# Kernel optimization log

Hardware: AMD Instinct MI355X
Metric: run time of the kernel (lower is better)

## Reference

```python
import jax, jax.numpy as jnp
import numpy as np

# pywt db8 reconstruction low-pass filter (rec_lo); other filters derived per pywt conventions
_REC_LO = np.array([
    0.05441584224308161, 0.3128715909144659, 0.6756307362980128,
    0.5853546836548691, -0.015829105256023893, -0.2840155429624281,
    0.00047248457399797254, 0.128747426620186, -0.01736930100202211,
    -0.04408825393106472, 0.013981027917015516, 0.008746094047015655,
    -0.00487035299301066, -0.0003917403729959771, 0.0006754494059985568,
    -0.00011747678400228192], dtype=np.float64)
_F = 16
_REC_HI = np.array([(-1.0) ** k * _REC_LO[_F - 1 - k] for k in range(_F)])  # qmf
_DEC_LO = _REC_LO[::-1].copy()
_DEC_HI = _REC_HI[::-1].copy()
# lax.conv does cross-correlation; np.convolve flips the filter, so pre-flip here
_DEC_K = np.ascontiguousarray(np.stack([_DEC_LO[::-1], _DEC_HI[::-1]])[:, None, :])  # [2,1,F]
_REC_K = np.ascontiguousarray(np.stack([_REC_LO[::-1], _REC_HI[::-1]])[None, :, :])  # [1,2,F]
_THRESHOLD_FACTOR = 1.0


def _dwt_last(x):
    # single-level DWT along last axis, pywt 'symmetric' boundary mode
    shp = x.shape
    xf = x.reshape(-1, 1, shp[-1])
    xe = jnp.pad(xf, ((0, 0), (0, 0), (_F - 1, _F - 1)), mode='symmetric')[:, :, 1:]
    y = jax.lax.conv_general_dilated(xe, jnp.asarray(_DEC_K, x.dtype), (2,), 'VALID',
                                     dimension_numbers=('NCW', 'OIW', 'NCW'))  # [M,2,n]
    n = y.shape[-1]  # n = floor((N + F - 1) / 2)
    return y[:, 0].reshape(shp[:-1] + (n,)), y[:, 1].reshape(shp[:-1] + (n,))


def _idwt_last(ca, cd, out_len):
    # single-level inverse DWT along last axis; out_len = 2*n - F + 2
    shp = ca.shape
    n = shp[-1]
    m = int(np.prod(shp[:-1]))
    u = jnp.zeros((m, 2, 2 * n), ca.dtype)
    u = u.at[:, 0, ::2].set(ca.reshape(m, n)).at[:, 1, ::2].set(cd.reshape(m, n))
    ue = jnp.pad(u, ((0, 0), (0, 0), (_F - 1, _F - 1)))
    y = jax.lax.conv_general_dilated(ue, jnp.asarray(_REC_K, ca.dtype), (1,), 'VALID',
                                     dimension_numbers=('NCW', 'OIW', 'NCW'))[:, 0]
    return y[:, _F - 2:_F - 2 + out_len].reshape(shp[:-1] + (out_len,))


def _forward(x):
    B, H, W, C = x.shape
    M = B * C
    xm = jnp.transpose(x, (0, 3, 1, 2)).reshape(M, H, W)
    # level-1 wavedec2: rows (W axis) then columns (H axis)
    lo, hi = _dwt_last(xm)                               # [M,H,nW]
    ll, lh = _dwt_last(jnp.swapaxes(lo, -1, -2))         # [M,nW,nH]
    hl, hh = _dwt_last(jnp.swapaxes(hi, -1, -2))         # [M,nW,nH]
    # universal threshold from median abs of all detail subbands, per sample/channel
    det = jnp.concatenate([lh.reshape(M, -1), hl.reshape(M, -1), hh.reshape(M, -1)], axis=-1)
    sigma = jnp.median(jnp.abs(det), axis=-1) / 0.6745
    t = (sigma * jnp.sqrt(2.0 * jnp.log(float(H * W))) * _THRESHOLD_FACTOR)[:, None, None]
    soft = lambda c: jnp.sign(c) * jnp.maximum(jnp.abs(c) - t, 0.0)
    lh, hl, hh = soft(lh), soft(hl), soft(hh)
    # waverec2: inverse along H then along W
    nH = ll.shape[-1]
    Hr = 2 * nH - _F + 2
    rl = jnp.swapaxes(_idwt_last(ll, lh, Hr), -1, -2)    # [M,Hr,nW]
    rh = jnp.swapaxes(_idwt_last(hl, hh, Hr), -1, -2)    # [M,Hr,nW]
    nW = rl.shape[-1]
    y = _idwt_last(rl, rh, 2 * nW - _F + 2)              # [M,Hr,Wr]
    y = y[:, :H, :W].reshape(B, C, H, W)
    return jnp.transpose(y, (0, 2, 3, 1)).astype(x.dtype)


def setup_inputs() -> dict:
    key = jax.random.key(0)
    x = jax.random.normal(key, (32, 512, 512, 3), dtype=jnp.float32)
    return {"x": x}


def reference(x):
    return _forward(x)
```

## Files before the change

kernel.cpp:

```cpp
#include <hip/hip_runtime.h>
#include <math.h>

#define B_   32
#define H_   512
#define W_   512
#define C_   3
#define M_   96
#define NW_  263
#define NH_  263
#define DETPER 69169
#define DETTOT 207507
#define DETSTRIDE 207508
#define NVEC 51876
#define KRANK  103753u

#define SXS 144
#define CR  12

#define CAP  32768
#define LCAP 4096

__device__ __constant__ float RLO[16] = {
    0.05441584224308161f,  0.3128715909144659f,   0.6756307362980128f,
    0.5853546836548691f,  -0.015829105256023893f, -0.2840155429624281f,
    0.00047248457399797254f, 0.128747426620186f,  -0.01736930100202211f,
   -0.04408825393106472f,  0.013981027917015516f,  0.008746094047015655f,
   -0.00487035299301066f, -0.0003917403729959771f, 0.0006754494059985568f,
   -0.00011747678400228192f};
__device__ __constant__ float RHI[16] = {
   -0.00011747678400228192f, -0.0006754494059985568f, -0.0003917403729959771f,
    0.00487035299301066f,     0.008746094047015655f,  -0.013981027917015516f,
   -0.04408825393106472f,     0.01736930100202211f,    0.128747426620186f,
   -0.00047248457399797254f, -0.2840155429624281f,     0.015829105256023893f,
    0.5853546836548691f,     -0.6756307362980128f,     0.3128715909144659f,
   -0.05441584224308161f};

__device__ __forceinline__ int refl(int q, int N) {
    if (q < 0)  return -q - 1;
    if (q >= N) return 2 * N - 1 - q;
    return q;
}

__device__ __forceinline__ float softthr(float v, float thr) {
    float a = fabsf(v) - thr;
    return a > 0.f ? copysignf(a, v) : 0.f;
}

__global__ __launch_bounds__(256) void k_zero(unsigned* __restrict__ p, int n) {
    int i = blockIdx.x * 256 + threadIdx.x;
    if (i < n) p[i] = 0u;
}

__global__ __launch_bounds__(256) void k_fwd(const float* __restrict__ x,
                                             float* __restrict__ ll,
                                             float* __restrict__ det,
                                             unsigned* __restrict__ hist) {
    __shared__ float sX[CR * SXS];
    __shared__ float sLO[46 * 64], sHI[46 * 64];
    __shared__ unsigned hh[2048];
    const int m   = blockIdx.x;
    const int jw0 = blockIdx.y * 64;
    const int jh0 = blockIdx.z * 16;
    const int b = m / 3, c = m - 3 * (m / 3);
    const int tid = threadIdx.x;
    const int prow0 = 2 * jh0 - 14, pcol0 = 2 * jw0 - 14;
    for (int i = tid; i < 2048; i += 256) hh[i] = 0u;
    for (int r0 = 0; r0 < 46; r0 += CR) {
        const int nr = (46 - r0) < CR ? (46 - r0) : CR;
        for (int l = tid; l < nr * 142; l += 256) {
            int rr = l / 142, cl = l - rr * 142;
            int h = refl(prow0 + r0 + rr, H_);
            int w = refl(pcol0 + cl, W_);
            sX[rr * SXS + cl] = x[((size_t)(b * H_ + h) * W_ + w) * C_ + c];
        }
        __syncthreads();
        for (int l = tid; l < nr * 64; l += 256) {
            int rr = l >> 6, j = l & 63;
            const float* px = &sX[rr * SXS + 2 * j];
            float al = 0.f, ah = 0.f;
#pragma unroll
            for (int k = 0; k < 16; ++k) {
                al = fmaf(px[k], RLO[k], al);
                ah = fmaf(px[k], RHI[k], ah);
            }
            sLO[(r0 + rr) * 64 + j] = al;
            sHI[(r0 + rr) * 64 + j] = ah;
        }
        __syncthreads();
    }
    const int tx = tid & 63, tg = tid >> 6;
    const int jw = jw0 + tx;
    const bool vw = (jw < NW_);
    float vl[22], vh[22];
#pragma unroll
    for (int s = 0; s < 22; ++s) {
        int row = 8 * tg + s;
        vl[s] = sLO[row * 64 + tx];
        vh[s] = sHI[row * 64 + tx];
    }
    float* llp = ll + (size_t)m * DETPER;
    float* dp  = det + (size_t)m * DETSTRIDE;
#pragma unroll
    for (int d = 0; d < 4; ++d) {
        int jh = jh0 + 4 * tg + d;
        float a0 = 0.f, a1 = 0.f, a2 = 0.f, a3 = 0.f;
#pragma unroll
        for (int k = 0; k < 16; ++k) {
            float fl = vl[2 * d + k], fh = vh[2 * d + k];
            a0 = fmaf(fl, RLO[k], a0);
            a1 = fmaf(fl, RHI[k], a1);
            a2 = fmaf(fh, RLO[k], a2);
            a3 = fmaf(fh, RHI[k], a3);
        }
        if (vw && jh < NH_) {
            size_t o = (size_t)jh * NW_ + jw;
            llp[o] = a0;
            dp[o] = a1;
            dp[DETPER + o] = a2;
            dp[2 * DETPER + o] = a3;
            atomicAdd(&hh[__float_as_uint(fabsf(a1)) >> 21], 1u);
            atomicAdd(&hh[__float_as_uint(fabsf(a2)) >> 21], 1u);
            atomicAdd(&hh[__float_as_uint(fabsf(a3)) >> 21], 1u);
        }
    }
    __syncthreads();
    for (int i = tid; i < 2048; i += 256)
        if (hh[i]) atomicAdd(&hist[m * 2048 + i], hh[i]);
}

__global__ __launch_bounds__(256) void k_hist2(const float* __restrict__ det,
                                               const int* __restrict__ selBin1,
                                               unsigned* __restrict__ hist,
                                               unsigned* __restrict__ cnt,
                                               unsigned* __restrict__ list,
                                               int docap) {
    __shared__ unsigned h[2048];
    __shared__ unsigned cbuf[LCAP];
    __shared__ unsigned ccnt, sbase;
    const int tid = threadIdx.x, m = blockIdx.x;
    const unsigned target = (unsigned)selBin1[m];
    for (int i = tid; i < 2048; i += 256) h[i] = 0u;
    if (tid == 0) ccnt = 0u;
    __syncthreads();
    const float* dp = det + (size_t)m * DETSTRIDE;
    const float4* dp4 = (const float4*)dp;
    const int stride = gridDim.y * 256;
    unsigned* const lst = list + (size_t)m * CAP;
    auto take = [&](unsigned u) {
        if ((u >> 21) == target) {
            atomicAdd(&h[(u >> 10) & 0x7FFu], 1u);
            if (docap) {
                unsigned p = atomicAdd(&ccnt, 1u);
                if (p < LCAP) cbuf[p] = u;
                else {
                    unsigned g = atomicAdd(&cnt[m], 1u);
                    if (g < CAP) lst[g] = u;
                }
            }
        }
    };
    for (int v = blockIdx.y * 256 + tid; v < NVEC; v += stride) {
        float4 f = dp4[v];
        take(__float_as_uint(fabsf(f.x)));
        take(__float_as_uint(fabsf(f.y)));
        take(__float_as_uint(fabsf(f.z)));
        take(__float_as_uint(fabsf(f.w)));
    }
    if (blockIdx.y == 0 && tid < DETTOT - 4 * NVEC)
        take(__float_as_uint(fabsf(dp[4 * NVEC + tid])));
    __syncthreads();
    if (docap) {
        unsigned n = ccnt < LCAP ? ccnt : LCAP;
        if (tid == 0) sbase = atomicAdd(&cnt[m], n);
        __syncthreads();
        for (unsigned i = tid; i < n; i += 256) {
            unsigned p = sbase + i;
            if (p < CAP) lst[p] = cbuf[i];
        }
    }
    for (int i = tid; i < 2048; i += 256)
        if (h[i]) atomicAdd(&hist[m * 2048 + i], h[i]);
}

__global__ __launch_bounds__(256) void k_hist3(const float* __restrict__ det,
                                               const int* __restrict__ selBin1,
                                               const int* __restrict__ selBin2,
                                               const unsigned* __restrict__ cnt,
                                               const unsigned* __restrict__ list,
                                               int docap,
                                               unsigned* __restrict__ hist) {
    __shared__ unsigned h[1024];
    const int tid = threadIdx.x, m = blockIdx.x;
    for (int i = tid; i < 1024; i += 256) h[i] = 0u;
    __syncthreads();
    const unsigned n = cnt[m];
    const bool fast = docap && (n <= CAP);
    if (fast) {
        const unsigned b2 = (unsigned)selBin2[m];
        const unsigned* lst = list + (size_t)m * CAP;
        const int stride = gridDim.y * 256;
        for (unsigned i = blockIdx.y * 256 + tid; i < n; i += stride) {
            unsigned u = lst[i];
            if (((u >> 10) & 0x7FFu) == b2) atomicAdd(&h[u & 0x3FFu], 1u);
        }
    } else {
        const unsigned target = ((unsigned)selBin1[m] << 11) | (unsigned)selBin2[m];
        const float* dp = det + (size_t)m * DETSTRIDE;
        const float4* dp4 = (const float4*)dp;
        const int stride = gridDim.y * 256;
        for (int v = blockIdx.y * 256 + tid; v < NVEC; v += stride) {
            float4 f = dp4[v];
            unsigned a = __float_as_uint(fabsf(f.x));
            unsigned b = __float_as_uint(fabsf(f.y));
            unsigned c = __float_as_uint(fabsf(f.z));
            unsigned d = __float_as_uint(fabsf(f.w));
            if ((a >> 10) == target) atomicAdd(&h[a & 0x3FFu], 1u);
            if ((b >> 10) == target) atomicAdd(&h[b & 0x3FFu], 1u);
            if ((c >> 10) == target) atomicAdd(&h[c & 0x3FFu], 1u);
            if ((d >> 10) == target) atomicAdd(&h[d & 0x3FFu], 1u);
        }
        if (blockIdx.y == 0 && tid < DETTOT - 4 * NVEC) {
            unsigned u = __float_as_uint(fabsf(dp[4 * NVEC + tid]));
            if ((u >> 10) == target) atomicAdd(&h[u & 0x3FFu], 1u);
        }
    }
    __syncthreads();
    for (int i = tid; i < 1024; i += 256)
        if (h[i]) atomicAdd(&hist[m * 1024 + i], h[i]);
}

__device__ int histSelect(unsigned* hist, int nb, unsigned rank, unsigned* rem) {
    __shared__ unsigned ps[256];
    __shared__ int s_bin;
    __shared__ unsigned s_rem;
    const int tid = threadIdx.x;
    if (tid == 0) { s_bin = 0; s_rem = 0; }
    const int per = nb >> 8;
    unsigned s = 0;
    for (int i = 0; i < per; ++i) s += hist[tid * per + i];
    ps[tid] = s;
    __syncthreads();
    for (int off = 1; off < 256; off <<= 1) {
        unsigned v = ps[tid];
        unsigned add = (tid >= off) ? ps[tid - off] : 0u;
        __syncthreads();
        ps[tid] = v + add;
        __syncthreads();
    }
    unsigned incl = ps[tid], excl = incl - s;
    if (rank >= excl && rank < incl) {
        unsigned cum = excl;
        for (int i = 0; i < per; ++i) {
            unsigned c = hist[tid * per + i];
            if (cum + c > rank) { s_bin = tid * per + i; s_rem = rank - cum; break; }
            cum += c;
        }
    }
    __syncthreads();
    int rbin = s_bin;
    unsigned rr = s_rem;
    __syncthreads();
    *rem = rr;
    return rbin;
}

__global__ __launch_bounds__(256) void k_sel2048(const unsigned* __restrict__ hist,
                                                 const unsigned* __restrict__ rankIn,
                                                 int* __restrict__ selBin,
                                                 unsigned* __restrict__ rankOut) {
    __shared__ unsigned h[2048];
    const int m = blockIdx.x, tid = threadIdx.x;
    for (int i = tid; i < 2048; i += 256) h[i] = hist[m * 2048 + i];
    __syncthreads();
    unsigned rank = rankIn ? rankIn[m] : KRANK;
    unsigned rem;
    int bin = histSelect(h, 2048, rank, &rem);
    if (tid == 0) { selBin[m] = bin; rankOut[m] = rem; }
}

__global__ __launch_bounds__(256) void k_sel3(const unsigned* __restrict__ hist,
                                              const unsigned* __restrict__ rankIn,
                                              const int* __restrict__ selBin1,
                                              const int* __restrict__ selBin2,
                                              float* __restrict__ tval) {
    __shared__ unsigned h[1024];
    const int m = blockIdx.x, tid = threadIdx.x;
    for (int i = tid; i < 1024; i += 256) h[i] = hist[m * 1024 + i];
    __syncthreads();
    unsigned rem;
    int low = histSelect(h, 1024, rankIn[m], &rem);
    if (tid == 0) {
        unsigned bits = ((unsigned)selBin1[m] << 21) | ((unsigned)selBin2[m] << 10) | (unsigned)low;
        double med = (double)__uint_as_float(bits);
        tval[m] = (float)(med / 0.6745 * 4.995327667046959);
    }
}

__global__ __launch_bounds__(256) void k_inv(const float* __restrict__ ll,
                                             const float* __restrict__ det,
                                             const float* __restrict__ tval,
                                             float* __restrict__ out) {
    __shared__ float sLL[23 * 40], sLH[23 * 40], sHL[23 * 40], sHH[23 * 40];
    __shared__ float sRL[32 * 40], sRH[32 * 40];
    const int m  = blockIdx.x;
    const int w0 = blockIdx.y * 64;
    const int t0 = blockIdx.z * 32;
    const int b = m / 3, c = m - 3 * (m / 3);
    const int tid = threadIdx.x;
    const float thr = tval[m];
    const int jW0 = w0 >> 1, s0 = t0 >> 1;
    const float* llp = ll + (size_t)m * DETPER;
    const float* dp  = det + (size_t)m * DETSTRIDE;
    for (int l = tid; l < 23 * 39; l += 256) {
        int rr = l / 39, cc = l - rr * 39;
        size_t o = (size_t)(s0 + rr) * NW_ + (jW0 + cc);
        int li = rr * 40 + cc;
        sLL[li] = llp[o];
        sLH[li] = softthr(dp[o], thr);
        sHL[li] = softthr(dp[DETPER + o], thr);
        sHH[li] = softthr(dp[2 * DETPER + o], thr);
    }
    __syncthreads();
    for (int l = tid; l < 32 * 39; l += 256) {
        int tr = l / 39, cc = l - tr * 39;
        int srow = tr >> 1, r = tr & 1;
        float aL = 0.f, aH = 0.f;
#pragma unroll
        for (int a = 0; a < 8; ++a) {
            int li = (srow + 7 - a) * 40 + cc;
            float wl = RLO[2 * a + r], wh = RHI[2 * a + r];
            aL = fmaf(sLL[li], wl, fmaf(sLH[li], wh, aL));
            aH = fmaf(sHL[li], wl, fmaf(sHH[li], wh, aH));
        }
        sRL[tr * 40 + cc] = aL;
        sRH[tr * 40 + cc] = aH;
    }
    __syncthreads();
    for (int l = tid; l < 32 * 64; l += 256) {
        int tr = l >> 6, wloc = l & 63;
        int r = wloc & 1, jb = (wloc >> 1) + 7;
        float acc = 0.f;
#pragma unroll
        for (int a = 0; a < 8; ++a) {
            int li = tr * 40 + jb - a;
            acc = fmaf(sRL[li], RLO[2 * a + r], fmaf(sRH[li], RHI[2 * a + r], acc));
        }
        out[((size_t)(b * H_ + (t0 + tr)) * W_ + (w0 + wloc)) * C_ + c] = acc;
    }
}

extern "C" void kernel_launch(void* const* d_in, const int* in_sizes, int n_in,
                              void* d_out, int out_size, void* d_ws, size_t ws_size,
                              hipStream_t stream) {
    const float* x = (const float*)d_in[0];
    float* out = (float*)d_out;

    char* ws = (char*)d_ws;
    float* ll  = (float*)ws; ws += (size_t)M_ * DETPER * 4;
    float* det = (float*)ws; ws += (size_t)M_ * DETSTRIDE * 4;
    unsigned* hist1 = (unsigned*)ws; ws += (size_t)M_ * 2048 * 4;
    unsigned* hist2 = (unsigned*)ws; ws += (size_t)M_ * 2048 * 4;
    unsigned* hist3 = (unsigned*)ws; ws += (size_t)M_ * 1024 * 4;
    unsigned* cnt   = (unsigned*)ws;   ws += M_ * 4;
    int*      selBin1 = (int*)ws;      ws += M_ * 4;
    int*      selBin2 = (int*)ws;      ws += M_ * 4;
    unsigned* rank1   = (unsigned*)ws; ws += M_ * 4;
    unsigned* rank2   = (unsigned*)ws; ws += M_ * 4;
    float*    tval    = (float*)ws;    ws += M_ * 4;
    unsigned* list    = (unsigned*)ws; ws += (size_t)M_ * CAP * 4;
    const int docap = (ws_size >= (size_t)((char*)(list + (size_t)M_ * CAP) - (char*)d_ws)) ? 1 : 0;

    const int histWords = M_ * (2048 + 2048 + 1024) + M_;
    k_zero   <<<dim3((histWords + 255) / 256), 256, 0, stream>>>(hist1, histWords);
    k_fwd    <<<dim3(M_, 5, 17),  256, 0, stream>>>(x, ll, det, hist1);
    k_sel2048<<<dim3(M_),         256, 0, stream>>>(hist1, nullptr, selBin1, rank1);
    k_hist2  <<<dim3(M_, 16),     256, 0, stream>>>(det, selBin1, hist2, cnt, list, docap);
    k_sel2048<<<dim3(M_),         256, 0, stream>>>(hist2, rank1, selBin2, rank2);
    k_hist3  <<<dim3(M_, 16),     256, 0, stream>>>(det, selBin1, selBin2, cnt, list, docap, hist3);
    k_sel3   <<<dim3(M_),         256, 0, stream>>>(hist3, rank2, selBin1, selBin2, tval);
    k_inv    <<<dim3(M_, 8, 16),  256, 0, stream>>>(ll, det, tval, out);
}
```

Before: 449.4 us.

## Split histogram out of forward DWT, use wave-aggregated list append, vectorize inverse

The first-pass histogram is moved out of the forward DWT kernel into a separate k_hist1 pass, so the forward kernel no longer does shared-memory atomics or carries a 2048-entry LDS histogram, at the cost of re-reading the detail coefficients. k_hist2 replaces its LDS staging buffer with a ballot/popcount wave-aggregated global append to the candidate list. The inverse kernel's two separable passes are restructured so each thread computes several outputs from float4 LDS reads and keeps data in registers, cutting LDS traffic and index arithmetic. The extra kernel launch and the extra read of detail data are the added cost.

```diff
diff --git a/kernel.cpp b/kernel.cpp
--- a/kernel.cpp
+++ b/kernel.cpp
@@ -18,7 +18,6 @@
 #define CR  12
 
 #define CAP  32768
-#define LCAP 4096
 
 __device__ __constant__ float RLO[16] = {
     0.05441584224308161f,  0.3128715909144659f,   0.6756307362980128f,
@@ -53,18 +52,15 @@
 
 __global__ __launch_bounds__(256) void k_fwd(const float* __restrict__ x,
                                              float* __restrict__ ll,
-                                             float* __restrict__ det,
-                                             unsigned* __restrict__ hist) {
+                                             float* __restrict__ det) {
     __shared__ float sX[CR * SXS];
     __shared__ float sLO[46 * 64], sHI[46 * 64];
-    __shared__ unsigned hh[2048];
     const int m   = blockIdx.x;
     const int jw0 = blockIdx.y * 64;
     const int jh0 = blockIdx.z * 16;
     const int b = m / 3, c = m - 3 * (m / 3);
     const int tid = threadIdx.x;
     const int prow0 = 2 * jh0 - 14, pcol0 = 2 * jw0 - 14;
-    for (int i = tid; i < 2048; i += 256) hh[i] = 0u;
     for (int r0 = 0; r0 < 46; r0 += CR) {
         const int nr = (46 - r0) < CR ? (46 - r0) : CR;
         for (int l = tid; l < nr * 142; l += 256) {
@@ -90,7 +86,7 @@
     }
     const int tx = tid & 63, tg = tid >> 6;
     const int jw = jw0 + tx;
-    const bool vw = (jw < NW_);
+    if (jw >= NW_) return;
     float vl[22], vh[22];
 #pragma unroll
     for (int s = 0; s < 22; ++s) {
@@ -103,6 +99,7 @@
 #pragma unroll
     for (int d = 0; d < 4; ++d) {
         int jh = jh0 + 4 * tg + d;
+        if (jh >= NH_) continue;
         float a0 = 0.f, a1 = 0.f, a2 = 0.f, a3 = 0.f;
 #pragma unroll
         for (int k = 0; k < 16; ++k) {
@@ -112,20 +109,37 @@
             a2 = fmaf(fh, RLO[k], a2);
             a3 = fmaf(fh, RHI[k], a3);
         }
-        if (vw && jh < NH_) {
-            size_t o = (size_t)jh * NW_ + jw;
-            llp[o] = a0;
-            dp[o] = a1;
-            dp[DETPER + o] = a2;
-            dp[2 * DETPER + o] = a3;
-            atomicAdd(&hh[__float_as_uint(fabsf(a1)) >> 21], 1u);
-            atomicAdd(&hh[__float_as_uint(fabsf(a2)) >> 21], 1u);
-            atomicAdd(&hh[__float_as_uint(fabsf(a3)) >> 21], 1u);
-        }
+        size_t o = (size_t)jh * NW_ + jw;
+        llp[o] = a0;
+        dp[o] = a1;
+        dp[DETPER + o] = a2;
+        dp[2 * DETPER + o] = a3;
+    }
+}
+
+__global__ __launch_bounds__(256) void k_hist1(const float* __restrict__ det,
+                                               unsigned* __restrict__ hist) {
+    __shared__ unsigned h[2048];
+    const int tid = threadIdx.x, m = blockIdx.x;
+    for (int i = tid; i < 2048; i += 256) h[i] = 0u;
+    __syncthreads();
+    const float* dp = det + (size_t)m * DETSTRIDE;
+    const float4* dp4 = (const float4*)dp;
+    const int stride = gridDim.y * 256;
+    for (int v = blockIdx.y * 256 + tid; v < NVEC; v += stride) {
+        float4 f = dp4[v];
+        atomicAdd(&h[__float_as_uint(fabsf(f.x)) >> 21], 1u);
+        atomicAdd(&h[__float_as_uint(fabsf(f.y)) >> 21], 1u);
+        atomicAdd(&h[__float_as_uint(fabsf(f.z)) >> 21], 1u);
+        atomicAdd(&h[__float_as_uint(fabsf(f.w)) >> 21], 1u);
+    }
+    if (blockIdx.y == 0 && tid < DETTOT - 4 * NVEC) {
+        unsigned u = __float_as_uint(fabsf(dp[4 * NVEC + tid]));
+        atomicAdd(&h[u >> 21], 1u);
     }
     __syncthreads();
     for (int i = tid; i < 2048; i += 256)
-        if (hh[i]) atomicAdd(&hist[m * 2048 + i], hh[i]);
+        if (h[i]) atomicAdd(&hist[m * 2048 + i], h[i]);
 }
 
 __global__ __launch_bounds__(256) void k_hist2(const float* __restrict__ det,
@@ -135,27 +149,28 @@
                                                unsigned* __restrict__ list,
                                                int docap) {
     __shared__ unsigned h[2048];
-    __shared__ unsigned cbuf[LCAP];
-    __shared__ unsigned ccnt, sbase;
     const int tid = threadIdx.x, m = blockIdx.x;
     const unsigned target = (unsigned)selBin1[m];
     for (int i = tid; i < 2048; i += 256) h[i] = 0u;
-    if (tid == 0) ccnt = 0u;
     __syncthreads();
     const float* dp = det + (size_t)m * DETSTRIDE;
     const float4* dp4 = (const float4*)dp;
     const int stride = gridDim.y * 256;
     unsigned* const lst = list + (size_t)m * CAP;
+    const unsigned lane = tid & 63;
     auto take = [&](unsigned u) {
-        if ((u >> 21) == target) {
-            atomicAdd(&h[(u >> 10) & 0x7FFu], 1u);
-            if (docap) {
-                unsigned p = atomicAdd(&ccnt, 1u);
-                if (p < LCAP) cbuf[p] = u;
-                else {
-                    unsigned g = atomicAdd(&cnt[m], 1u);
-                    if (g < CAP) lst[g] = u;
-                }
+        bool pred = ((u >> 21) == target);
+        if (pred) atomicAdd(&h[(u >> 10) & 0x7FFu], 1u);
+        if (docap) {
+            unsigned long long mask = __ballot(pred);
+            if (pred) {
+                unsigned off = (unsigned)__popcll(mask & ((1ull << lane) - 1ull));
+                int leader = __ffsll((unsigned long long)mask) - 1;
+                unsigned base = 0u;
+                if ((int)lane == leader) base = atomicAdd(&cnt[m], (unsigned)__popcll(mask));
+                base = (unsigned)__shfl((int)base, leader, 64);
+                unsigned p = base + off;
+                if (p < CAP) lst[p] = u;
             }
         }
     };
@@ -169,15 +184,6 @@
     if (blockIdx.y == 0 && tid < DETTOT - 4 * NVEC)
         take(__float_as_uint(fabsf(dp[4 * NVEC + tid])));
     __syncthreads();
-    if (docap) {
-        unsigned n = ccnt < LCAP ? ccnt : LCAP;
-        if (tid == 0) sbase = atomicAdd(&cnt[m], n);
-        __syncthreads();
-        for (unsigned i = tid; i < n; i += 256) {
-            unsigned p = sbase + i;
-            if (p < CAP) lst[p] = cbuf[i];
-        }
-    }
     for (int i = tid; i < 2048; i += 256)
         if (h[i]) atomicAdd(&hist[m * 2048 + i], h[i]);
 }
@@ -321,31 +327,63 @@
         sHH[li] = softthr(dp[2 * DETPER + o], thr);
     }
     __syncthreads();
-    for (int l = tid; l < 32 * 39; l += 256) {
-        int tr = l / 39, cc = l - tr * 39;
-        int srow = tr >> 1, r = tr & 1;
-        float aL = 0.f, aH = 0.f;
+    for (int l = tid; l < 160; l += 256) {
+        int s = l / 10, q = l - 10 * (l / 10);
+        float4 aL0 = make_float4(0.f, 0.f, 0.f, 0.f), aL1 = aL0, aH0 = aL0, aH1 = aL0;
 #pragma unroll
         for (int a = 0; a < 8; ++a) {
-            int li = (srow + 7 - a) * 40 + cc;
-            float wl = RLO[2 * a + r], wh = RHI[2 * a + r];
-            aL = fmaf(sLL[li], wl, fmaf(sLH[li], wh, aL));
-            aH = fmaf(sHL[li], wl, fmaf(sHH[li], wh, aH));
-        }
-        sRL[tr * 40 + cc] = aL;
-        sRH[tr * 40 + cc] = aH;
-    }
-    __syncthreads();
-    for (int l = tid; l < 32 * 64; l += 256) {
-        int tr = l >> 6, wloc = l & 63;
-        int r = wloc & 1, jb = (wloc >> 1) + 7;
-        float acc = 0.f;
-#pragma unroll
-        for (int a = 0; a < 8; ++a) {
-            int li = tr * 40 + jb - a;
-            acc = fmaf(sRL[li], RLO[2 * a + r], fmaf(sRH[li], RHI[2 * a + r], acc));
-        }
-        out[((size_t)(b * H_ + (t0 + tr)) * W_ + (w0 + wloc)) * C_ + c] = acc;
+            int li = (s + 7 - a) * 40 + 4 * q;
+            float4 vLL = *(const float4*)&sLL[li];
+            float4 vLH = *(const float4*)&sLH[li];
+            float4 vHL = *(const float4*)&sHL[li];
+            float4 vHH = *(const float4*)&sHH[li];
+            float w00 = RLO[2 * a],     h00 = RHI[2 * a];
+            float w01 = RLO[2 * a + 1], h01 = RHI[2 * a + 1];
+            aL0.x = fmaf(vLL.x, w00, fmaf(vLH.x, h00, aL0.x));
+            aL0.y = fmaf(vLL.y, w00, fmaf(vLH.y, h00, aL0.y));
+            aL0.z = fmaf(vLL.z, w00, fmaf(vLH.z, h00, aL0.z));
+            aL0.w = fmaf(vLL.w, w00, fmaf(vLH.w, h00, aL0.w));
+            aL1.x = fmaf(vLL.x, w01, fmaf(vLH.x, h01, aL1.x));
+            aL1.y = fmaf(vLL.y, w01, fmaf(vLH.y, h01, aL1.y));
+            aL1.z = fmaf(vLL.z, w01, fmaf(vLH.z, h01, aL1.z));
+            aL1.w = fmaf(vLL.w, w01, fmaf(vLH.w, h01, aL1.w));
+            aH0.x = fmaf(vHL.x, w00, fmaf(vHH.x, h00, aH0.x));
+            aH0.y = fmaf(vHL.y, w00, fmaf(vHH.y, h00, aH0.y));
+            aH0.z = fmaf(vHL.z, w00, fmaf(vHH.z, h00, aH0.z));
+            aH0.w = fmaf(vHL.w, w00, fmaf(vHH.w, h00, aH0.w));
+            aH1.x = fmaf(vHL.x, w01, fmaf(vHH.x, h01, aH1.x));
+            aH1.y = fmaf(vHL.y, w01, fmaf(vHH.y, h01, aH1.y));
+            aH1.z = fmaf(vHL.z, w01, fmaf(vHH.z, h01, aH1.z));
+            aH1.w = fmaf(vHL.w, w01, fmaf(vHH.w, h01, aH1.w));
+        }
+        *(float4*)&sRL[(2 * s) * 40 + 4 * q]     = aL0;
+        *(float4*)&sRL[(2 * s + 1) * 40 + 4 * q] = aL1;
+        *(float4*)&sRH[(2 * s) * 40 + 4 * q]     = aH0;
+        *(float4*)&sRH[(2 * s + 1) * 40 + 4 * q] = aH1;
+    }
+    __syncthreads();
+    {
+        const int tr = tid >> 3, jg = tid & 7;
+        const float4* pl = (const float4*)&sRL[tr * 40 + 4 * jg];
+        const float4* ph = (const float4*)&sRH[tr * 40 + 4 * jg];
+        float4 L0 = pl[0], L1 = pl[1], L2 = pl[2];
+        float4 K0 = ph[0], K1 = ph[1], K2 = ph[2];
+        float rl[12] = {L0.x,L0.y,L0.z,L0.w, L1.x,L1.y,L1.z,L1.w, L2.x,L2.y,L2.z,L2.w};
+        float rh[12] = {K0.x,K0.y,K0.z,K0.w, K1.x,K1.y,K1.z,K1.w, K2.x,K2.y,K2.z,K2.w};
+        size_t obase = ((size_t)(b * H_ + (t0 + tr)) * W_ + (w0 + 8 * jg)) * C_ + c;
+#pragma unroll
+        for (int u = 0; u < 4; ++u) {
+#pragma unroll
+            for (int r = 0; r < 2; ++r) {
+                float acc = 0.f;
+#pragma unroll
+                for (int a = 0; a < 8; ++a) {
+                    int sdx = u + 7 - a;
+                    acc = fmaf(rl[sdx], RLO[2 * a + r], fmaf(rh[sdx], RHI[2 * a + r], acc));
+                }
+                out[obase + (size_t)(2 * u + r) * C_] = acc;
+            }
+        }
     }
 }
 
@@ -372,7 +410,8 @@
 
     const int histWords = M_ * (2048 + 2048 + 1024) + M_;
     k_zero   <<<dim3((histWords + 255) / 256), 256, 0, stream>>>(hist1, histWords);
-    k_fwd    <<<dim3(M_, 5, 17),  256, 0, stream>>>(x, ll, det, hist1);
+    k_fwd    <<<dim3(M_, 5, 17),  256, 0, stream>>>(x, ll, det);
+    k_hist1  <<<dim3(M_, 16),     256, 0, stream>>>(det, hist1);
     k_sel2048<<<dim3(M_),         256, 0, stream>>>(hist1, nullptr, selBin1, rank1);
     k_hist2  <<<dim3(M_, 16),     256, 0, stream>>>(det, selBin1, hist2, cnt, list, docap);
     k_sel2048<<<dim3(M_),         256, 0, stream>>>(hist2, rank1, selBin2, rank2);
```

Result: slower. 1.436 ms (+219.4%).

## Use per-thread candidate slots in radix select and trim forward edge tiles

Applied to the files above, without the earlier changes.

The radix-select candidate list moves from shared-memory atomic compaction to per-thread strided slots with a per-thread count and an overflow flag. k_hist3 then scans each thread's own slot instead of a global compacted list, which removes the shared and global atomics on the append path. k_fwd adds a light path for the last column tile that loads and filters only the few columns it needs, reuses sX as the histogram buffer to save LDS, and raises the row chunk size to 16. In exchange, the list buffer grows larger and a per-thread count array is written, and any overflowing sample falls back to a full rescan.

```diff
diff --git a/kernel.cpp b/kernel.cpp
--- a/kernel.cpp
+++ b/kernel.cpp
@@ -15,10 +15,11 @@
 #define KRANK  103753u
 
 #define SXS 144
-#define CR  12
-
-#define CAP  32768
-#define LCAP 4096
+#define CR  16
+
+#define NBY   16
+#define SLOTS 4096
+#define SCAP  24
 
 __device__ __constant__ float RLO[16] = {
     0.05441584224308161f,  0.3128715909144659f,   0.6756307362980128f,
@@ -57,37 +58,65 @@
                                              unsigned* __restrict__ hist) {
     __shared__ float sX[CR * SXS];
     __shared__ float sLO[46 * 64], sHI[46 * 64];
-    __shared__ unsigned hh[2048];
+    unsigned* hh = (unsigned*)sX;
     const int m   = blockIdx.x;
     const int jw0 = blockIdx.y * 64;
     const int jh0 = blockIdx.z * 16;
     const int b = m / 3, c = m - 3 * (m / 3);
     const int tid = threadIdx.x;
     const int prow0 = 2 * jh0 - 14, pcol0 = 2 * jw0 - 14;
+    const bool light = (jw0 + 64 > NW_);
+    if (!light) {
+        for (int r0 = 0; r0 < 46; r0 += CR) {
+            const int nr = (46 - r0) < CR ? (46 - r0) : CR;
+            for (int l = tid; l < nr * 142; l += 256) {
+                int rr = l / 142, cl = l - rr * 142;
+                int h = refl(prow0 + r0 + rr, H_);
+                int w = refl(pcol0 + cl, W_);
+                sX[rr * SXS + cl] = x[((size_t)(b * H_ + h) * W_ + w) * C_ + c];
+            }
+            __syncthreads();
+            for (int l = tid; l < nr * 64; l += 256) {
+                int rr = l >> 6, j = l & 63;
+                const float* px = &sX[rr * SXS + 2 * j];
+                float al = 0.f, ah = 0.f;
+#pragma unroll
+                for (int k = 0; k < 16; ++k) {
+                    al = fmaf(px[k], RLO[k], al);
+                    ah = fmaf(px[k], RHI[k], ah);
+                }
+                sLO[(r0 + rr) * 64 + j] = al;
+                sHI[(r0 + rr) * 64 + j] = ah;
+            }
+            __syncthreads();
+        }
+    } else {
+        for (int r0 = 0; r0 < 46; r0 += CR) {
+            const int nr = (46 - r0) < CR ? (46 - r0) : CR;
+            for (int l = tid; l < nr * 28; l += 256) {
+                int rr = l / 28, cl = l - rr * 28;
+                int h = refl(prow0 + r0 + rr, H_);
+                int w = refl(pcol0 + cl, W_);
+                sX[rr * SXS + cl] = x[((size_t)(b * H_ + h) * W_ + w) * C_ + c];
+            }
+            __syncthreads();
+            for (int l = tid; l < nr * 7; l += 256) {
+                int rr = l / 7, j = l - 7 * (l / 7);
+                const float* px = &sX[rr * SXS + 2 * j];
+                float al = 0.f, ah = 0.f;
+#pragma unroll
+                for (int k = 0; k < 16; ++k) {
+                    al = fmaf(px[k], RLO[k], al);
+                    ah = fmaf(px[k], RHI[k], ah);
+                }
+                sLO[(r0 + rr) * 64 + j] = al;
+                sHI[(r0 + rr) * 64 + j] = ah;
+            }
+            __syncthreads();
+        }
+    }
     for (int i = tid; i < 2048; i += 256) hh[i] = 0u;
-    for (int r0 = 0; r0 < 46; r0 += CR) {
-        const int nr = (46 - r0) < CR ? (46 - r0) : CR;
-        for (int l = tid; l < nr * 142; l += 256) {
-            int rr = l / 142, cl = l - rr * 142;
-            int h = refl(prow0 + r0 + rr, H_);
-            int w = refl(pcol0 + cl, W_);
-            sX[rr * SXS + cl] = x[((size_t)(b * H_ + h) * W_ + w) * C_ + c];
-        }
-        __syncthreads();
-        for (int l = tid; l < nr * 64; l += 256) {
-            int rr = l >> 6, j = l & 63;
-            const float* px = &sX[rr * SXS + 2 * j];
-            float al = 0.f, ah = 0.f;
-#pragma unroll
-            for (int k = 0; k < 16; ++k) {
-                al = fmaf(px[k], RLO[k], al);
-                ah = fmaf(px[k], RHI[k], ah);
-            }
-            sLO[(r0 + rr) * 64 + j] = al;
-            sHI[(r0 + rr) * 64 + j] = ah;
-        }
-        __syncthreads();
-    }
+    __syncthreads();
     const int tx = tid & 63, tg = tid >> 6;
     const int jw = jw0 + tx;
     const bool vw = (jw < NW_);
@@ -132,52 +161,43 @@
                                                const int* __restrict__ selBin1,
                                                unsigned* __restrict__ hist,
                                                unsigned* __restrict__ cnt,
+                                               unsigned* __restrict__ ovf,
                                                unsigned* __restrict__ list,
                                                int docap) {
     __shared__ unsigned h[2048];
-    __shared__ unsigned cbuf[LCAP];
-    __shared__ unsigned ccnt, sbase;
-    const int tid = threadIdx.x, m = blockIdx.x;
+    const int tid = threadIdx.x, m = blockIdx.x, by = blockIdx.y;
     const unsigned target = (unsigned)selBin1[m];
     for (int i = tid; i < 2048; i += 256) h[i] = 0u;
-    if (tid == 0) ccnt = 0u;
     __syncthreads();
     const float* dp = det + (size_t)m * DETSTRIDE;
     const float4* dp4 = (const float4*)dp;
     const int stride = gridDim.y * 256;
-    unsigned* const lst = list + (size_t)m * CAP;
+    const unsigned slot = (unsigned)(by * 256 + tid);
+    unsigned* const lst = list + (size_t)m * SLOTS * SCAP;
+    unsigned mycnt = 0u;
     auto take = [&](unsigned u) {
         if ((u >> 21) == target) {
             atomicAdd(&h[(u >> 10) & 0x7FFu], 1u);
             if (docap) {
-                unsigned p = atomicAdd(&ccnt, 1u);
-                if (p < LCAP) cbuf[p] = u;
-                else {
-                    unsigned g = atomicAdd(&cnt[m], 1u);
-                    if (g < CAP) lst[g] = u;
-                }
+                if (mycnt < SCAP) lst[mycnt * SLOTS + slot] = u;
+                ++mycnt;
             }
         }
     };
-    for (int v = blockIdx.y * 256 + tid; v < NVEC; v += stride) {
+    for (int v = by * 256 + tid; v < NVEC; v += stride) {
         float4 f = dp4[v];
         take(__float_as_uint(fabsf(f.x)));
         take(__float_as_uint(fabsf(f.y)));
         take(__float_as_uint(fabsf(f.z)));
         take(__float_as_uint(fabsf(f.w)));
     }
-    if (blockIdx.y == 0 && tid < DETTOT - 4 * NVEC)
+    if (by == 0 && tid < DETTOT - 4 * NVEC)
         take(__float_as_uint(fabsf(dp[4 * NVEC + tid])));
-    __syncthreads();
     if (docap) {
-        unsigned n = ccnt < LCAP ? ccnt : LCAP;
-        if (tid == 0) sbase = atomicAdd(&cnt[m], n);
-        __syncthreads();
-        for (unsigned i = tid; i < n; i += 256) {
-            unsigned p = sbase + i;
-            if (p < CAP) lst[p] = cbuf[i];
-        }
-    }
+        cnt[m * SLOTS + slot] = mycnt;
+        if (mycnt > SCAP) atomicOr(&ovf[m], 1u);
+    }
+    __syncthreads();
     for (int i = tid; i < 2048; i += 256)
         if (h[i]) atomicAdd(&hist[m * 2048 + i], h[i]);
 }
@@ -186,21 +206,22 @@
                                                const int* __restrict__ selBin1,
                                                const int* __restrict__ selBin2,
                                                const unsigned* __restrict__ cnt,
+                                               const unsigned* __restrict__ ovf,
                                                const unsigned* __restrict__ list,
                                                int docap,
                                                unsigned* __restrict__ hist) {
     __shared__ unsigned h[1024];
-    const int tid = threadIdx.x, m = blockIdx.x;
+    const int tid = threadIdx.x, m = blockIdx.x, by = blockIdx.y;
     for (int i = tid; i < 1024; i += 256) h[i] = 0u;
     __syncthreads();
-    const unsigned n = cnt[m];
-    const bool fast = docap && (n <= CAP);
+    const bool fast = docap && (ovf[m] == 0u);
     if (fast) {
         const unsigned b2 = (unsigned)selBin2[m];
-        const unsigned* lst = list + (size_t)m * CAP;
-        const int stride = gridDim.y * 256;
-        for (unsigned i = blockIdx.y * 256 + tid; i < n; i += stride) {
-            unsigned u = lst[i];
+        const unsigned slot = (unsigned)(by * 256 + tid);
+        const unsigned n = cnt[m * SLOTS + slot];
+        const unsigned* lst = list + (size_t)m * SLOTS * SCAP;
+        for (unsigned j = 0; j < n; ++j) {
+            unsigned u = lst[j * SLOTS + slot];
             if (((u >> 10) & 0x7FFu) == b2) atomicAdd(&h[u & 0x3FFu], 1u);
         }
     } else {
@@ -208,7 +229,7 @@
         const float* dp = det + (size_t)m * DETSTRIDE;
         const float4* dp4 = (const float4*)dp;
         const int stride = gridDim.y * 256;
-        for (int v = blockIdx.y * 256 + tid; v < NVEC; v += stride) {
+        for (int v = by * 256 + tid; v < NVEC; v += stride) {
             float4 f = dp4[v];
             unsigned a = __float_as_uint(fabsf(f.x));
             unsigned b = __float_as_uint(fabsf(f.y));
@@ -219,7 +240,7 @@
             if ((c >> 10) == target) atomicAdd(&h[c & 0x3FFu], 1u);
             if ((d >> 10) == target) atomicAdd(&h[d & 0x3FFu], 1u);
         }
-        if (blockIdx.y == 0 && tid < DETTOT - 4 * NVEC) {
+        if (by == 0 && tid < DETTOT - 4 * NVEC) {
             unsigned u = __float_as_uint(fabsf(dp[4 * NVEC + tid]));
             if ((u >> 10) == target) atomicAdd(&h[u & 0x3FFu], 1u);
         }
@@ -361,22 +382,23 @@
     unsigned* hist1 = (unsigned*)ws; ws += (size_t)M_ * 2048 * 4;
     unsigned* hist2 = (unsigned*)ws; ws += (size_t)M_ * 2048 * 4;
     unsigned* hist3 = (unsigned*)ws; ws += (size_t)M_ * 1024 * 4;
-    unsigned* cnt   = (unsigned*)ws;   ws += M_ * 4;
+    unsigned* ovf   = (unsigned*)ws;   ws += M_ * 4;
     int*      selBin1 = (int*)ws;      ws += M_ * 4;
     int*      selBin2 = (int*)ws;      ws += M_ * 4;
     unsigned* rank1   = (unsigned*)ws; ws += M_ * 4;
     unsigned* rank2   = (unsigned*)ws; ws += M_ * 4;
     float*    tval    = (float*)ws;    ws += M_ * 4;
-    unsigned* list    = (unsigned*)ws; ws += (size_t)M_ * CAP * 4;
-    const int docap = (ws_size >= (size_t)((char*)(list + (size_t)M_ * CAP) - (char*)d_ws)) ? 1 : 0;
+    unsigned* cnt     = (unsigned*)ws; ws += (size_t)M_ * SLOTS * 4;
+    unsigned* list    = (unsigned*)ws; ws += (size_t)M_ * SLOTS * SCAP * 4;
+    const int docap = (ws_size >= (size_t)(ws - (char*)d_ws)) ? 1 : 0;
 
     const int histWords = M_ * (2048 + 2048 + 1024) + M_;
     k_zero   <<<dim3((histWords + 255) / 256), 256, 0, stream>>>(hist1, histWords);
     k_fwd    <<<dim3(M_, 5, 17),  256, 0, stream>>>(x, ll, det, hist1);
     k_sel2048<<<dim3(M_),         256, 0, stream>>>(hist1, nullptr, selBin1, rank1);
-    k_hist2  <<<dim3(M_, 16),     256, 0, stream>>>(det, selBin1, hist2, cnt, list, docap);
+    k_hist2  <<<dim3(M_, NBY),    256, 0, stream>>>(det, selBin1, hist2, cnt, ovf, list, docap);
     k_sel2048<<<dim3(M_),         256, 0, stream>>>(hist2, rank1, selBin2, rank2);
-    k_hist3  <<<dim3(M_, 16),     256, 0, stream>>>(det, selBin1, selBin2, cnt, list, docap, hist3);
+    k_hist3  <<<dim3(M_, NBY),    256, 0, stream>>>(det, selBin1, selBin2, cnt, ovf, list, docap, hist3);
     k_sel3   <<<dim3(M_),         256, 0, stream>>>(hist3, rank2, selBin1, selBin2, tval);
     k_inv    <<<dim3(M_, 8, 16),  256, 0, stream>>>(ll, det, tval, out);
 }
```

After: 447.2 us. Within noise of the previous version (-0.5%).
